# Kernel tuning notes

Hardware: AMD Instinct MI355X
Metric: run time of the kernel (lower is better)

## Reference

```python
import jax, jax.numpy as jnp
import numpy as np


def _gru_cell(x, h, W_ih, W_hh, b_ih, b_hh):
    # torch.nn.GRUCell math. x: [T,H], h: [T,H]; W_*: [3H,H]; b_*: [3H]
    gi = x @ W_ih.T + b_ih          # [T,3H]
    gh = h @ W_hh.T + b_hh          # [T,3H]
    i_r, i_z, i_n = jnp.split(gi, 3, axis=-1)
    h_r, h_z, h_n = jnp.split(gh, 3, axis=-1)
    r = jax.nn.sigmoid(i_r + h_r)
    z = jax.nn.sigmoid(i_z + h_z)
    n = jnp.tanh(i_n + r * h_n)
    return (1.0 - z) * n + z * h


def setup_inputs() -> dict:
    key = jax.random.key(0)
    ks = jax.random.split(key, 7)
    S, T, H = 65536, 8192, 1024
    bound = 1.0 / np.sqrt(H)  # torch GRUCell init scale
    return {
        "speaker_memory": jax.random.normal(ks[0], (S, H), dtype=jnp.float32),
        "speaker_ids": jax.random.randint(ks[1], (T,), 0, S, dtype=jnp.int32),
        "edu_reps": jax.random.normal(ks[2], (T, H), dtype=jnp.float32),
        "W_ih": jax.random.uniform(ks[3], (3 * H, H), jnp.float32, -bound, bound),
        "W_hh": jax.random.uniform(ks[4], (3 * H, H), jnp.float32, -bound, bound),
        "b_ih": jax.random.uniform(ks[5], (3 * H,), jnp.float32, -bound, bound),
        "b_hh": jax.random.uniform(ks[6], (3 * H,), jnp.float32, -bound, bound),
    }


def reference(speaker_memory, speaker_ids, edu_reps, W_ih, W_hh, b_ih, b_hh):
    # The torch loop reads h from the ORIGINAL speaker_memory for every step,
    # so all T GRU updates are independent; for duplicate speaker ids the last
    S, H = speaker_memory.shape
    T = speaker_ids.shape[0]
    h = speaker_memory[speaker_ids]                      # [T,H] gather
    new_h = _gru_cell(edu_reps, h, W_ih, W_hh, b_ih, b_hh)  # [T,H]
    # last occurrence position of each speaker id (int min for untouched ids)
    last_pos = jax.ops.segment_max(jnp.arange(T), speaker_ids, num_segments=S)
    touched = last_pos >= 0                              # [S]
    gathered = new_h[jnp.clip(last_pos, 0, T - 1)]       # [S,H]
    return jnp.where(touched[:, None], gathered, speaker_memory)
```

## Files before the change

kernel.cpp:

```cpp
#include <hip/hip_runtime.h>
#include <hip/hip_bf16.h>
#include <stdint.h>
#include <stddef.h>

typedef short short8 __attribute__((ext_vector_type(8)));
typedef float f32x4 __attribute__((ext_vector_type(4)));

#define SROWS 65536
#define TROWS 8192
#define HDIM  1024
#define KDIM  2048
#define NT    32
#define BUF   57344

__device__ __forceinline__ unsigned short f2bf(float f) {
  union { float f; uint32_t u; } v; v.f = f;
  uint32_t u = v.u;
  uint32_t r = (u + 0x7FFFu + ((u >> 16) & 1u)) >> 16;
  return (unsigned short)r;
}

__device__ __forceinline__ float fast_sigmoid(float x) {
  return __builtin_amdgcn_rcpf(1.0f + __builtin_amdgcn_exp2f(-1.44269504f * x));
}
__device__ __forceinline__ float fast_tanh(float x) {
  return 1.0f - 2.0f * __builtin_amdgcn_rcpf(1.0f + __builtin_amdgcn_exp2f(2.88539008f * x));
}


__global__ __launch_bounds__(256) void k_initlp(int* lp) {
  int i = blockIdx.x * 256 + threadIdx.x;
  if (i < SROWS) lp[i] = -1;
}

__global__ __launch_bounds__(256) void k_lp(const int* __restrict__ sid, int* lp) {
  int i = blockIdx.x * 256 + threadIdx.x;
  if (i < TROWS) atomicMax(&lp[sid[i]], i);
}

__global__ __launch_bounds__(256) void k_flags(const int* __restrict__ lp,
                                               unsigned long long* __restrict__ flagb) {
  int i = blockIdx.x * 256 + threadIdx.x;
  unsigned long long m = __ballot(lp[i] < 0);
  if ((threadIdx.x & 63) == 0) flagb[i >> 6] = m;
}

__global__ __launch_bounds__(256) void k_bias(const float* __restrict__ bih,
                                              const float* __restrict__ bhh,
                                              float* __restrict__ btab) {
  int j = blockIdx.x * 256 + threadIdx.x;
  if (j < HDIM) {
    btab[4*j+0] = bih[j] + bhh[j];
    btab[4*j+1] = bih[j+HDIM] + bhh[j+HDIM];
    btab[4*j+2] = bih[j+2*HDIM];
    btab[4*j+3] = bhh[j+2*HDIM];
  }
}

__global__ __launch_bounds__(256) void k_build_A(const float* __restrict__ edu,
                                                 const float* __restrict__ mem,
                                                 const int* __restrict__ sid,
                                                 unsigned short* __restrict__ Ac) {
  const int idx = blockIdx.x * 256 + threadIdx.x;
  const int t  = idx >> 8;
  const int k0 = (idx & 255) << 3;
  const float* src;
  if (k0 < HDIM) src = edu + (size_t)t * HDIM + k0;
  else           src = mem + (size_t)sid[t] * HDIM + (k0 - HDIM);
  f32x4 f0 = *(const f32x4*)src;
  f32x4 f1 = *(const f32x4*)(src + 4);
  short8 v;
  v[0]=(short)f2bf(f0[0]); v[1]=(short)f2bf(f0[1]); v[2]=(short)f2bf(f0[2]); v[3]=(short)f2bf(f0[3]);
  v[4]=(short)f2bf(f1[0]); v[5]=(short)f2bf(f1[1]); v[6]=(short)f2bf(f1[2]); v[7]=(short)f2bf(f1[3]);
  *(short8*)(Ac + (size_t)idx * 8) = v;
}

__global__ __launch_bounds__(256) void k_build_B2(const float* __restrict__ Wih,
                                                  const float* __restrict__ Whh,
                                                  unsigned short* __restrict__ Brz,
                                                  unsigned short* __restrict__ Bn) {
  const int idx = blockIdx.x * 256 + threadIdx.x;
  const int c  = idx >> 8;
  const int k0 = (idx & 255) << 3;
  const float* src;
  unsigned short* dst;
  if (c < 2048) {
    const int j = c >> 1, g = c & 1;
    const int row = j + g * 1024;
    src = (k0 < HDIM) ? Wih + (size_t)row * HDIM + k0
                      : Whh + (size_t)row * HDIM + (k0 - HDIM);
    dst = Brz + (size_t)c * KDIM + k0;
  } else {
    const int j = c - 2048;
    src = (k0 < HDIM) ? Wih + (size_t)(j + 2*HDIM) * HDIM + k0
                      : Whh + (size_t)(j + 2*HDIM) * HDIM + (k0 - HDIM);
    dst = Bn + (size_t)j * KDIM + k0;
  }
  f32x4 f0 = *(const f32x4*)src;
  f32x4 f1 = *(const f32x4*)(src + 4);
  short8 v;
  v[0]=(short)f2bf(f0[0]); v[1]=(short)f2bf(f0[1]); v[2]=(short)f2bf(f0[2]); v[3]=(short)f2bf(f0[3]);
  v[4]=(short)f2bf(f1[0]); v[5]=(short)f2bf(f1[1]); v[6]=(short)f2bf(f1[2]); v[7]=(short)f2bf(f1[3]);
  *(short8*)dst = v;
}


#define FENCE() asm volatile("" ::: "memory")
#define BAR()   __builtin_amdgcn_s_barrier()
#define LGKM0() asm volatile("s_waitcnt lgkmcnt(0)" ::: "memory")
#define VM(N)   asm volatile("s_waitcnt vmcnt(" #N ")" ::: "memory")

#define STAGE(p0, p1, ldsoff)                                                              \
  __builtin_amdgcn_global_load_lds((const __attribute__((address_space(1))) void*)(p0),   \
      (__attribute__((address_space(3))) void*)(smem + (ldsoff) + w * 1024), 16, 0, 0);    \
  __builtin_amdgcn_global_load_lds((const __attribute__((address_space(1))) void*)(p1),   \
      (__attribute__((address_space(3))) void*)(smem + (ldsoff) + 8192 + w * 1024), 16, 0, 0);

#define STAGE1(p0, ldsoff)                                                                 \
  __builtin_amdgcn_global_load_lds((const __attribute__((address_space(1))) void*)(p0),   \
      (__attribute__((address_space(3))) void*)(smem + (ldsoff) + w * 1024), 16, 0, 0);

#define LDF(base, frag, koff) (*(const short8*)(smem + (base) + (size_t)(frag) * 2048 + (koff)))

#define MF(a, b, c) __builtin_amdgcn_mfma_f32_16x16x32_bf16(a, b, c, 0, 0, 0)

#define PHASE(m0, STAGE_STMT, TAIL, ACCN)                                     \
  {                                                                           \
    short8 af0a = LDF(abase, (m0),     foff0);                                \
    short8 af0b = LDF(abase, (m0),     foff1);                                \
    short8 af1a = LDF(abase, (m0) + 1, foff0);                                \
    short8 af1b = LDF(abase, (m0) + 1, foff1);                                \
    STAGE_STMT;                                                               \
    FENCE(); BAR();                                                           \
    LGKM0();                                                                  \
    __builtin_amdgcn_s_setprio(1);                                            \
    acc_rz[(m0)][0]   = MF(af0a, bf[0][0], acc_rz[(m0)][0]);                  \
    acc_rz[(m0)][0]   = MF(af0b, bf[0][1], acc_rz[(m0)][0]);                  \
    acc_rz[(m0)][1]   = MF(af0a, bf[1][0], acc_rz[(m0)][1]);                  \
    acc_rz[(m0)][1]   = MF(af0b, bf[1][1], acc_rz[(m0)][1]);                  \
    ACCN[(m0)]        = MF(af0a, bf[2][0], ACCN[(m0)]);                       \
    ACCN[(m0)]        = MF(af0b, bf[2][1], ACCN[(m0)]);                       \
    acc_rz[(m0)+1][0] = MF(af1a, bf[0][0], acc_rz[(m0)+1][0]);                \
    acc_rz[(m0)+1][0] = MF(af1b, bf[0][1], acc_rz[(m0)+1][0]);                \
    acc_rz[(m0)+1][1] = MF(af1a, bf[1][0], acc_rz[(m0)+1][1]);                \
    acc_rz[(m0)+1][1] = MF(af1b, bf[1][1], acc_rz[(m0)+1][1]);                \
    ACCN[(m0)+1]      = MF(af1a, bf[2][0], ACCN[(m0)+1]);                     \
    ACCN[(m0)+1]      = MF(af1b, bf[2][1], ACCN[(m0)+1]);                     \
    __builtin_amdgcn_s_setprio(0);                                            \
    TAIL;                                                                     \
    FENCE(); BAR();                                                           \
  }

#define COPY_TAIL                                                             \
  {                                                                           \
    VM(3);                                                                    \
    const int rr0 = 4 * t + ccp, rr1 = rr0 + 2;                               \
    const unsigned long long fwt = (t < 16) ? fw0 : fw1;                      \
    const bool nv0 = (fwt >> (rr0 & 63)) & 1ull;                              \
    const bool nv1 = (fwt >> (rr1 & 63)) & 1ull;                              \
    if ((t & 1) == 0) {                                                       \
      if (vY0) __builtin_nontemporal_store(cpY0, (f32x4*)&out[(size_t)sY0 * HDIM + ccol]); \
      if (vY1) __builtin_nontemporal_store(cpY1, (f32x4*)&out[(size_t)sY1 * HDIM + ccol]); \
      vX0 = nv0; vX1 = nv1; sX0 = cbase + rr0; sX1 = cbase + rr1;             \
      if (vX0) cpX0 = __builtin_nontemporal_load((const f32x4*)&mem[(size_t)sX0 * HDIM + ccol]); \
      if (vX1) cpX1 = __builtin_nontemporal_load((const f32x4*)&mem[(size_t)sX1 * HDIM + ccol]); \
    } else {                                                                  \
      if (vX0) __builtin_nontemporal_store(cpX0, (f32x4*)&out[(size_t)sX0 * HDIM + ccol]); \
      if (vX1) __builtin_nontemporal_store(cpX1, (f32x4*)&out[(size_t)sX1 * HDIM + ccol]); \
      vY0 = nv0; vY1 = nv1; sY0 = cbase + rr0; sY1 = cbase + rr1;             \
      if (vY0) cpY0 = __builtin_nontemporal_load((const f32x4*)&mem[(size_t)sY0 * HDIM + ccol]); \
      if (vY1) cpY1 = __builtin_nontemporal_load((const f32x4*)&mem[(size_t)sY1 * HDIM + ccol]); \
    }                                                                         \
  }

#define TILE_BODY(ACCN)                                                       \
  {                                                                           \
    const int cur = t & 1, nxt = cur ^ 1;                                     \
    const size_t buf = (size_t)cur * BUF, nbuf = (size_t)nxt * BUF;           \
    const size_t abase  = buf + (size_t)wm * 16384;                           \
    const size_t rzbase = buf + 32768 + (size_t)wn * 4096;                    \
    const size_t nbase  = buf + 49152 + (size_t)wn * 2048;                    \
    const int kt1 = (t + 1 < NT) ? t + 1 : NT - 1;                            \
    const int kt2 = (t + 2 < NT) ? t + 2 : NT - 1;                            \
    short8 bf[3][2];                                                          \
    bf[0][0] = LDF(rzbase, 0, foff0); bf[0][1] = LDF(rzbase, 0, foff1);       \
    bf[1][0] = LDF(rzbase, 1, foff0); bf[1][1] = LDF(rzbase, 1, foff1);       \
    bf[2][0] = LDF(nbase,  0, foff0); bf[2][1] = LDF(nbase,  0, foff1);       \
    PHASE(0, STAGE(pA0r0 + kt1 * 64, pA0r1 + kt1 * 64, nbuf), ;, ACCN)        \
    PHASE(2, STAGE(pA1r0 + kt1 * 64, pA1r1 + kt1 * 64, nbuf + 16384), ;, ACCN)\
    PHASE(4, STAGE(pRZ0 + kt2 * 64, pRZ1 + kt2 * 64, buf + 32768), ;, ACCN)   \
    PHASE(6, STAGE1(pN + kt2 * 64, buf + 49152), COPY_TAIL, ACCN)             \
  }

__global__ __launch_bounds__(512, 2)
void k_gru8(const unsigned short* __restrict__ Ac,
            const unsigned short* __restrict__ Brz,
            const unsigned short* __restrict__ Bn,
            const float* __restrict__ mem,
            const int* __restrict__ sid,
            const int* __restrict__ lp,
            const unsigned long long* __restrict__ flagb,
            const float* __restrict__ btab,
            float* __restrict__ out) {
  extern __shared__ char smem[];

  const int tid  = threadIdx.x;
  const int lane = tid & 63;
  const int w    = tid >> 6;
  const int wm   = w >> 2;
  const int wn   = w & 3;
  const int l15  = lane & 15;
  const int l4   = lane >> 4;

  const int bid = blockIdx.x;
  const int swz = (bid & 7) * 64 + (bid >> 3);
  const int t0  = (swz >> 4) * 256;
  const int j0  = (swz & 15) * 64;
  const int rz0 = j0 * 2;

  const int srow0 = tid >> 3;
  const int srow1 = 64 + srow0;
  const int scol  = ((tid & 7) * 8) ^ (((tid >> 3) & 7) << 3);

  const unsigned short* pA0r0 = Ac + (size_t)(t0 +       srow0) * KDIM + scol;
  const unsigned short* pA0r1 = Ac + (size_t)(t0 +       srow1) * KDIM + scol;
  const unsigned short* pA1r0 = Ac + (size_t)(t0 + 128 + srow0) * KDIM + scol;
  const unsigned short* pA1r1 = Ac + (size_t)(t0 + 128 + srow1) * KDIM + scol;
  const unsigned short* pRZ0  = Brz + (size_t)(rz0 + srow0) * KDIM + scol;
  const unsigned short* pRZ1  = Brz + (size_t)(rz0 + srow1) * KDIM + scol;
  const unsigned short* pN    = Bn  + (size_t)(j0  + srow0) * KDIM + scol;

  const int rsw = (l15 & 7) << 4;
  const size_t foff0 = (size_t)l15 * 128 + ((l4 * 16)      ^ rsw);
  const size_t foff1 = (size_t)l15 * 128 + ((64 + l4 * 16) ^ rsw);

  f32x4 acc_rz[8][2], acc_nlo[8], acc_nhi[8];
#pragma unroll
  for (int i = 0; i < 8; i++) {
    acc_rz[i][0] = (f32x4){0.f,0.f,0.f,0.f};
    acc_rz[i][1] = (f32x4){0.f,0.f,0.f,0.f};
    acc_nlo[i]   = (f32x4){0.f,0.f,0.f,0.f};
    acc_nhi[i]   = (f32x4){0.f,0.f,0.f,0.f};
  }

  const int cbase = bid << 7;
  const unsigned long long fw0 = flagb[bid * 2];
  const unsigned long long fw1 = flagb[bid * 2 + 1];
  const int ccp  = tid >> 8;
  const int ccol = (tid & 255) << 2;
  f32x4 cpX0, cpX1, cpY0, cpY1;
  bool  vX0 = false, vX1 = false, vY0 = false, vY1 = false;
  int   sX0 = 0, sX1 = 0, sY0 = 0, sY1 = 0;

  STAGE(pA0r0, pA0r1, 0);
  STAGE(pA1r0, pA1r1, 16384);
  STAGE(pRZ0, pRZ1, 32768);
  STAGE1(pN, 49152);
  STAGE(pRZ0 + 64, pRZ1 + 64, BUF + 32768);
  STAGE1(pN + 64, BUF + 49152);
  VM(3);
  FENCE(); BAR();

  for (int t = 0; t < 16; ++t) TILE_BODY(acc_nlo)
  for (int t = 16; t < NT; ++t) TILE_BODY(acc_nhi)

  VM(0);
  if (vY0) __builtin_nontemporal_store(cpY0, (f32x4*)&out[(size_t)sY0 * HDIM + ccol]);
  if (vY1) __builtin_nontemporal_store(cpY1, (f32x4*)&out[(size_t)sY1 * HDIM + ccol]);
  __syncthreads();
  float* epi = (float*)smem;
  const int jfirst = j0 + wn * 16 + l4 * 4;

#pragma unroll
  for (int mf = 0; mf < 8; mf++) {
#pragma unroll
    for (int f = 0; f < 2; f++)
#pragma unroll
      for (int r = 0; r < 4; r++)
        epi[w * 1088 + (l4 * 4 + r) * 68 + (f * 8 + (l15 >> 1)) * 4 + (l15 & 1)] = acc_rz[mf][f][r];
#pragma unroll
    for (int r = 0; r < 4; r++) {
      epi[w * 1088 + (l4 * 4 + r) * 68 + l15 * 4 + 2] = acc_nlo[mf][r];
      epi[w * 1088 + (l4 * 4 + r) * 68 + l15 * 4 + 3] = acc_nhi[mf][r];
    }
    __syncthreads();

    const int trow = t0 + wm * 128 + mf * 16 + l15;
    const int s    = sid[trow];
    const bool wr  = (lp[s] == trow);

    f32x4 q[4];
#pragma unroll
    for (int jj = 0; jj < 4; jj++)
      q[jj] = *(const f32x4*)&epi[w * 1088 + l15 * 68 + l4 * 16 + jj * 4];

    f32x4 hv = *(const f32x4*)&mem[(size_t)s * HDIM + jfirst];
    f32x4 o;
#pragma unroll
    for (int jj = 0; jj < 4; jj++) {
      const int j = jfirst + jj;
      f32x4 bt = *(const f32x4*)&btab[4 * j];
      float rr = fast_sigmoid(q[jj][0] + bt[0]);
      float zz = fast_sigmoid(q[jj][1] + bt[1]);
      float nn = fast_tanh(q[jj][2] + bt[2] + rr * (q[jj][3] + bt[3]));
      o[jj] = (1.0f - zz) * nn + zz * hv[jj];
    }
    if (wr) __builtin_nontemporal_store(o, (f32x4*)&out[(size_t)s * HDIM + jfirst]);
    __syncthreads();
  }
}


extern "C" void kernel_launch(void* const* d_in, const int* in_sizes, int n_in,
                              void* d_out, int out_size, void* d_ws, size_t ws_size,
                              hipStream_t stream) {
  const float* mem = (const float*)d_in[0];
  const int*   sid = (const int*)d_in[1];
  const float* edu = (const float*)d_in[2];
  const float* Wih = (const float*)d_in[3];
  const float* Whh = (const float*)d_in[4];
  const float* bih = (const float*)d_in[5];
  const float* bhh = (const float*)d_in[6];
  float* out = (float*)d_out;

  char* p = (char*)d_ws;
  unsigned short* Ac  = (unsigned short*)p; p += (size_t)TROWS * KDIM * 2;
  unsigned short* Brz = (unsigned short*)p; p += (size_t)2048 * KDIM * 2;
  unsigned short* Bn  = (unsigned short*)p; p += (size_t)1024 * KDIM * 2;
  int*   lp   = (int*)p;   p += (size_t)SROWS * 4;
  float* btab = (float*)p; p += (size_t)HDIM * 4 * 4;
  unsigned long long* flagb = (unsigned long long*)p; p += (size_t)(SROWS / 64) * 8;

  hipFuncSetAttribute((const void*)k_gru8, hipFuncAttributeMaxDynamicSharedMemorySize, 2 * BUF);

  hipLaunchKernelGGL(k_initlp, dim3(SROWS / 256), dim3(256), 0, stream, lp);
  hipLaunchKernelGGL(k_lp, dim3(TROWS / 256), dim3(256), 0, stream, sid, lp);
  hipLaunchKernelGGL(k_flags, dim3(SROWS / 256), dim3(256), 0, stream, lp, flagb);
  hipLaunchKernelGGL(k_bias, dim3(4), dim3(256), 0, stream, bih, bhh, btab);
  hipLaunchKernelGGL(k_build_A, dim3((TROWS * KDIM / 8) / 256), dim3(256), 0, stream, edu, mem, sid, Ac);
  hipLaunchKernelGGL(k_build_B2, dim3(3072), dim3(256), 0, stream, Wih, Whh, Brz, Bn);
  hipLaunchKernelGGL(k_gru8, dim3(512), dim3(512), 2 * BUF, stream,
                     Ac, Brz, Bn, mem, sid, lp, flagb, btab, out);
}
```

Before: 207.4 us.

## Halve GRU GEMM tile rows to double grid size and raise occupancy

Measured after the change: 209.6 us. No clear change (+1.1%).

```diff
diff --git a/kernel.cpp b/kernel.cpp
--- a/kernel.cpp
+++ b/kernel.cpp
@@ -11,7 +11,7 @@
 #define HDIM  1024
 #define KDIM  2048
 #define NT    32
-#define BUF   57344
+#define BUF   40960
 
 __device__ __forceinline__ unsigned short f2bf(float f) {
   union { float f; uint32_t u; } v; v.f = f;
@@ -107,7 +107,8 @@
 
 #define FENCE() asm volatile("" ::: "memory")
 #define BAR()   __builtin_amdgcn_s_barrier()
-#define LGKM0() asm volatile("s_waitcnt lgkmcnt(0)" ::: "memory")
+#define LGKM0() do { asm volatile("s_waitcnt lgkmcnt(0)" ::: "memory"); \
+                     __builtin_amdgcn_sched_barrier(0); } while (0)
 #define VM(N)   asm volatile("s_waitcnt vmcnt(" #N ")" ::: "memory")
 
 #define STAGE(p0, p1, ldsoff)                                                              \
@@ -124,75 +125,77 @@
 
 #define MF(a, b, c) __builtin_amdgcn_mfma_f32_16x16x32_bf16(a, b, c, 0, 0, 0)
 
-#define PHASE(m0, STAGE_STMT, TAIL, ACCN)                                     \
-  {                                                                           \
-    short8 af0a = LDF(abase, (m0),     foff0);                                \
-    short8 af0b = LDF(abase, (m0),     foff1);                                \
-    short8 af1a = LDF(abase, (m0) + 1, foff0);                                \
-    short8 af1b = LDF(abase, (m0) + 1, foff1);                                \
-    STAGE_STMT;                                                               \
-    FENCE(); BAR();                                                           \
-    LGKM0();                                                                  \
-    __builtin_amdgcn_s_setprio(1);                                            \
-    acc_rz[(m0)][0]   = MF(af0a, bf[0][0], acc_rz[(m0)][0]);                  \
-    acc_rz[(m0)][0]   = MF(af0b, bf[0][1], acc_rz[(m0)][0]);                  \
-    acc_rz[(m0)][1]   = MF(af0a, bf[1][0], acc_rz[(m0)][1]);                  \
-    acc_rz[(m0)][1]   = MF(af0b, bf[1][1], acc_rz[(m0)][1]);                  \
-    ACCN[(m0)]        = MF(af0a, bf[2][0], ACCN[(m0)]);                       \
-    ACCN[(m0)]        = MF(af0b, bf[2][1], ACCN[(m0)]);                       \
-    acc_rz[(m0)+1][0] = MF(af1a, bf[0][0], acc_rz[(m0)+1][0]);                \
-    acc_rz[(m0)+1][0] = MF(af1b, bf[0][1], acc_rz[(m0)+1][0]);                \
-    acc_rz[(m0)+1][1] = MF(af1a, bf[1][0], acc_rz[(m0)+1][1]);                \
-    acc_rz[(m0)+1][1] = MF(af1b, bf[1][1], acc_rz[(m0)+1][1]);                \
-    ACCN[(m0)+1]      = MF(af1a, bf[2][0], ACCN[(m0)+1]);                     \
-    ACCN[(m0)+1]      = MF(af1b, bf[2][1], ACCN[(m0)+1]);                     \
-    __builtin_amdgcn_s_setprio(0);                                            \
-    TAIL;                                                                     \
-    FENCE(); BAR();                                                           \
-  }
-
-#define COPY_TAIL                                                             \
-  {                                                                           \
-    VM(3);                                                                    \
-    const int rr0 = 4 * t + ccp, rr1 = rr0 + 2;                               \
-    const unsigned long long fwt = (t < 16) ? fw0 : fw1;                      \
-    const bool nv0 = (fwt >> (rr0 & 63)) & 1ull;                              \
-    const bool nv1 = (fwt >> (rr1 & 63)) & 1ull;                              \
-    if ((t & 1) == 0) {                                                       \
-      if (vY0) __builtin_nontemporal_store(cpY0, (f32x4*)&out[(size_t)sY0 * HDIM + ccol]); \
-      if (vY1) __builtin_nontemporal_store(cpY1, (f32x4*)&out[(size_t)sY1 * HDIM + ccol]); \
-      vX0 = nv0; vX1 = nv1; sX0 = cbase + rr0; sX1 = cbase + rr1;             \
-      if (vX0) cpX0 = __builtin_nontemporal_load((const f32x4*)&mem[(size_t)sX0 * HDIM + ccol]); \
-      if (vX1) cpX1 = __builtin_nontemporal_load((const f32x4*)&mem[(size_t)sX1 * HDIM + ccol]); \
-    } else {                                                                  \
-      if (vX0) __builtin_nontemporal_store(cpX0, (f32x4*)&out[(size_t)sX0 * HDIM + ccol]); \
-      if (vX1) __builtin_nontemporal_store(cpX1, (f32x4*)&out[(size_t)sX1 * HDIM + ccol]); \
-      vY0 = nv0; vY1 = nv1; sY0 = cbase + rr0; sY1 = cbase + rr1;             \
-      if (vY0) cpY0 = __builtin_nontemporal_load((const f32x4*)&mem[(size_t)sY0 * HDIM + ccol]); \
-      if (vY1) cpY1 = __builtin_nontemporal_load((const f32x4*)&mem[(size_t)sY1 * HDIM + ccol]); \
-    }                                                                         \
-  }
+#define MFMA12(ACCN)                                                          \
+    acc_rz[0][0] = MF(af[0], bf0, acc_rz[0][0]);                              \
+    acc_rz[0][1] = MF(af[0], bf1, acc_rz[0][1]);                              \
+    ACCN[0]      = MF(af[0], bf2, ACCN[0]);                                   \
+    acc_rz[1][0] = MF(af[1], bf0, acc_rz[1][0]);                              \
+    acc_rz[1][1] = MF(af[1], bf1, acc_rz[1][1]);                              \
+    ACCN[1]      = MF(af[1], bf2, ACCN[1]);                                   \
+    acc_rz[2][0] = MF(af[2], bf0, acc_rz[2][0]);                              \
+    acc_rz[2][1] = MF(af[2], bf1, acc_rz[2][1]);                              \
+    ACCN[2]      = MF(af[2], bf2, ACCN[2]);                                   \
+    acc_rz[3][0] = MF(af[3], bf0, acc_rz[3][0]);                              \
+    acc_rz[3][1] = MF(af[3], bf1, acc_rz[3][1]);                              \
+    ACCN[3]      = MF(af[3], bf2, ACCN[3]);
 
 #define TILE_BODY(ACCN)                                                       \
   {                                                                           \
-    const int cur = t & 1, nxt = cur ^ 1;                                     \
-    const size_t buf = (size_t)cur * BUF, nbuf = (size_t)nxt * BUF;           \
-    const size_t abase  = buf + (size_t)wm * 16384;                           \
-    const size_t rzbase = buf + 32768 + (size_t)wn * 4096;                    \
-    const size_t nbase  = buf + 49152 + (size_t)wn * 2048;                    \
+    const int cur = t & 1;                                                    \
+    const size_t buf = (size_t)cur * BUF, nbuf = (size_t)(cur ^ 1) * BUF;     \
+    const size_t abase  = buf + (size_t)wm * 8192;                            \
+    const size_t rzbase = buf + 16384 + (size_t)wn * 4096;                    \
+    const size_t nbase  = buf + 32768 + (size_t)wn * 2048;                    \
     const int kt1 = (t + 1 < NT) ? t + 1 : NT - 1;                            \
-    const int kt2 = (t + 2 < NT) ? t + 2 : NT - 1;                            \
-    short8 bf[3][2];                                                          \
-    bf[0][0] = LDF(rzbase, 0, foff0); bf[0][1] = LDF(rzbase, 0, foff1);       \
-    bf[1][0] = LDF(rzbase, 1, foff0); bf[1][1] = LDF(rzbase, 1, foff1);       \
-    bf[2][0] = LDF(nbase,  0, foff0); bf[2][1] = LDF(nbase,  0, foff1);       \
-    PHASE(0, STAGE(pA0r0 + kt1 * 64, pA0r1 + kt1 * 64, nbuf), ;, ACCN)        \
-    PHASE(2, STAGE(pA1r0 + kt1 * 64, pA1r1 + kt1 * 64, nbuf + 16384), ;, ACCN)\
-    PHASE(4, STAGE(pRZ0 + kt2 * 64, pRZ1 + kt2 * 64, buf + 32768), ;, ACCN)   \
-    PHASE(6, STAGE1(pN + kt2 * 64, buf + 49152), COPY_TAIL, ACCN)             \
-  }
-
-__global__ __launch_bounds__(512, 2)
+                  \
+    STAGE(pA0 + kt1 * 64, pA1 + kt1 * 64, nbuf);                              \
+    STAGE(pRZ0 + kt1 * 64, pRZ1 + kt1 * 64, nbuf + 16384);                    \
+    STAGE1(pN + kt1 * 64, nbuf + 32768);                                      \
+    VM(5);                                                                    \
+    FENCE(); BAR(); FENCE();                                                  \
+    {                                                                         \
+      short8 bf0 = LDF(rzbase, 0, foff0);                                     \
+      short8 bf1 = LDF(rzbase, 1, foff0);                                     \
+      short8 bf2 = LDF(nbase,  0, foff0);                                     \
+      short8 af[4];                                                           \
+      af[0] = LDF(abase, 0, foff0); af[1] = LDF(abase, 1, foff0);             \
+      af[2] = LDF(abase, 2, foff0); af[3] = LDF(abase, 3, foff0);             \
+      LGKM0();                                                                \
+      __builtin_amdgcn_s_setprio(1);                                          \
+      MFMA12(ACCN)                                                            \
+      __builtin_amdgcn_s_setprio(0);                                          \
+    }                                                                         \
+                    \
+    {                                                                         \
+      short8 bf0 = LDF(rzbase, 0, foff1);                                     \
+      short8 bf1 = LDF(rzbase, 1, foff1);                                     \
+      short8 bf2 = LDF(nbase,  0, foff1);                                     \
+      short8 af[4];                                                           \
+      af[0] = LDF(abase, 0, foff1); af[1] = LDF(abase, 1, foff1);             \
+      af[2] = LDF(abase, 2, foff1); af[3] = LDF(abase, 3, foff1);             \
+      LGKM0();                                                                \
+      __builtin_amdgcn_s_setprio(1);                                          \
+      MFMA12(ACCN)                                                            \
+      __builtin_amdgcn_s_setprio(0);                                          \
+    }                                                                         \
+    VM(5);                                                                    \
+    {                                                                         \
+      const int rr = 2 * t + ccp;                                             \
+      const bool nv = (fw >> rr) & 1ull;                                      \
+      if ((t & 1) == 0) {                                                     \
+        if (vY) __builtin_nontemporal_store(cpY, (f32x4*)&out[(size_t)sY * HDIM + ccol]); \
+        vX = nv; sX = cbase + rr;                                             \
+        if (vX) cpX = __builtin_nontemporal_load((const f32x4*)&mem[(size_t)sX * HDIM + ccol]); \
+      } else {                                                                \
+        if (vX) __builtin_nontemporal_store(cpX, (f32x4*)&out[(size_t)sX * HDIM + ccol]); \
+        vY = nv; sY = cbase + rr;                                             \
+        if (vY) cpY = __builtin_nontemporal_load((const f32x4*)&mem[(size_t)sY * HDIM + ccol]); \
+      }                                                                       \
+    }                                                                         \
+    FENCE(); BAR(); FENCE();                                                  \
+  }
+
+__global__ __launch_bounds__(512, 4)
 void k_gru8(const unsigned short* __restrict__ Ac,
             const unsigned short* __restrict__ Brz,
             const unsigned short* __restrict__ Bn,
@@ -213,66 +216,58 @@
   const int l4   = lane >> 4;
 
   const int bid = blockIdx.x;
-  const int swz = (bid & 7) * 64 + (bid >> 3);
-  const int t0  = (swz >> 4) * 256;
+  const int swz = (bid & 7) * 128 + (bid >> 3);
+  const int t0  = (swz >> 4) * 128;
   const int j0  = (swz & 15) * 64;
   const int rz0 = j0 * 2;
 
   const int srow0 = tid >> 3;
-  const int srow1 = 64 + srow0;
   const int scol  = ((tid & 7) * 8) ^ (((tid >> 3) & 7) << 3);
 
-  const unsigned short* pA0r0 = Ac + (size_t)(t0 +       srow0) * KDIM + scol;
-  const unsigned short* pA0r1 = Ac + (size_t)(t0 +       srow1) * KDIM + scol;
-  const unsigned short* pA1r0 = Ac + (size_t)(t0 + 128 + srow0) * KDIM + scol;
-  const unsigned short* pA1r1 = Ac + (size_t)(t0 + 128 + srow1) * KDIM + scol;
-  const unsigned short* pRZ0  = Brz + (size_t)(rz0 + srow0) * KDIM + scol;
-  const unsigned short* pRZ1  = Brz + (size_t)(rz0 + srow1) * KDIM + scol;
-  const unsigned short* pN    = Bn  + (size_t)(j0  + srow0) * KDIM + scol;
+  const unsigned short* pA0  = Ac  + (size_t)(t0 +       srow0) * KDIM + scol;
+  const unsigned short* pA1  = Ac  + (size_t)(t0 + 64 +  srow0) * KDIM + scol;
+  const unsigned short* pRZ0 = Brz + (size_t)(rz0 +      srow0) * KDIM + scol;
+  const unsigned short* pRZ1 = Brz + (size_t)(rz0 + 64 + srow0) * KDIM + scol;
+  const unsigned short* pN   = Bn  + (size_t)(j0  +      srow0) * KDIM + scol;
 
   const int rsw = (l15 & 7) << 4;
   const size_t foff0 = (size_t)l15 * 128 + ((l4 * 16)      ^ rsw);
   const size_t foff1 = (size_t)l15 * 128 + ((64 + l4 * 16) ^ rsw);
 
-  f32x4 acc_rz[8][2], acc_nlo[8], acc_nhi[8];
-#pragma unroll
-  for (int i = 0; i < 8; i++) {
+  f32x4 acc_rz[4][2], acc_nlo[4], acc_nhi[4];
+#pragma unroll
+  for (int i = 0; i < 4; i++) {
     acc_rz[i][0] = (f32x4){0.f,0.f,0.f,0.f};
     acc_rz[i][1] = (f32x4){0.f,0.f,0.f,0.f};
     acc_nlo[i]   = (f32x4){0.f,0.f,0.f,0.f};
     acc_nhi[i]   = (f32x4){0.f,0.f,0.f,0.f};
   }
 
-  const int cbase = bid << 7;
-  const unsigned long long fw0 = flagb[bid * 2];
-  const unsigned long long fw1 = flagb[bid * 2 + 1];
+  const int cbase = bid << 6;
+  const unsigned long long fw = flagb[bid];
   const int ccp  = tid >> 8;
   const int ccol = (tid & 255) << 2;
-  f32x4 cpX0, cpX1, cpY0, cpY1;
-  bool  vX0 = false, vX1 = false, vY0 = false, vY1 = false;
-  int   sX0 = 0, sX1 = 0, sY0 = 0, sY1 = 0;
-
-  STAGE(pA0r0, pA0r1, 0);
-  STAGE(pA1r0, pA1r1, 16384);
-  STAGE(pRZ0, pRZ1, 32768);
-  STAGE1(pN, 49152);
-  STAGE(pRZ0 + 64, pRZ1 + 64, BUF + 32768);
-  STAGE1(pN + 64, BUF + 49152);
-  VM(3);
-  FENCE(); BAR();
+  f32x4 cpX, cpY;
+  bool  vX = false, vY = false;
+  int   sX = 0, sY = 0;
+
+  STAGE(pA0, pA1, 0);
+  STAGE(pRZ0, pRZ1, 16384);
+  STAGE1(pN, 32768);
+  VM(0);
+  FENCE(); BAR(); FENCE();
 
   for (int t = 0; t < 16; ++t) TILE_BODY(acc_nlo)
   for (int t = 16; t < NT; ++t) TILE_BODY(acc_nhi)
 
   VM(0);
-  if (vY0) __builtin_nontemporal_store(cpY0, (f32x4*)&out[(size_t)sY0 * HDIM + ccol]);
-  if (vY1) __builtin_nontemporal_store(cpY1, (f32x4*)&out[(size_t)sY1 * HDIM + ccol]);
+  if (vY) __builtin_nontemporal_store(cpY, (f32x4*)&out[(size_t)sY * HDIM + ccol]);
   __syncthreads();
   float* epi = (float*)smem;
   const int jfirst = j0 + wn * 16 + l4 * 4;
 
 #pragma unroll
-  for (int mf = 0; mf < 8; mf++) {
+  for (int mf = 0; mf < 4; mf++) {
 #pragma unroll
     for (int f = 0; f < 2; f++)
 #pragma unroll
@@ -285,7 +280,7 @@
     }
     __syncthreads();
 
-    const int trow = t0 + wm * 128 + mf * 16 + l15;
+    const int trow = t0 + wm * 64 + mf * 16 + l15;
     const int s    = sid[trow];
     const bool wr  = (lp[s] == trow);
 
@@ -339,6 +334,6 @@
   hipLaunchKernelGGL(k_bias, dim3(4), dim3(256), 0, stream, bih, bhh, btab);
   hipLaunchKernelGGL(k_build_A, dim3((TROWS * KDIM / 8) / 256), dim3(256), 0, stream, edu, mem, sid, Ac);
   hipLaunchKernelGGL(k_build_B2, dim3(3072), dim3(256), 0, stream, Wih, Whh, Brz, Bn);
-  hipLaunchKernelGGL(k_gru8, dim3(512), dim3(512), 2 * BUF, stream,
+  hipLaunchKernelGGL(k_gru8, dim3(1024), dim3(512), 2 * BUF, stream,
                      Ac, Brz, Bn, mem, sid, lp, flagb, btab, out);
 }
```
